# Performance work log

Hardware: AMD Instinct MI355X
Metric: run time of the kernel (lower is better)

## Reference

```python
import jax, jax.numpy as jnp
import numpy as np

N_NODES = 100000
N_EDGES = 3200000
F_IN = 512
HIDDEN = 16
N_CLASSES = 7


def setup_inputs() -> dict:
    key = jax.random.key(0)
    k = jax.random.split(key, 6)
    x = jax.random.normal(k[0], (N_NODES, F_IN), dtype=jnp.float32)
    edge_index = jax.random.randint(k[1], (2, N_EDGES), 0, N_NODES, dtype=jnp.int32)
    W1 = jax.random.normal(k[2], (F_IN, HIDDEN), dtype=jnp.float32) / np.sqrt(F_IN)
    b1 = jnp.zeros((HIDDEN,), dtype=jnp.float32)
    W2 = jax.random.normal(k[3], (HIDDEN, N_CLASSES), dtype=jnp.float32) / np.sqrt(HIDDEN)
    b2 = jnp.zeros((N_CLASSES,), dtype=jnp.float32)
    return {"x": x, "edge_index": edge_index, "W1": W1, "b1": b1, "W2": W2, "b2": b2}


def _gcn_norm(edge_index, num_nodes):
    # gcn_norm with add_self_loops=True, edge_weight=None (all ones).
    loops = jnp.arange(num_nodes, dtype=edge_index.dtype)
    row = jnp.concatenate([edge_index[0], loops])  # source
    col = jnp.concatenate([edge_index[1], loops])  # target
    w = jnp.ones(row.shape[0], dtype=jnp.float32)
    deg = jax.ops.segment_sum(w, col, num_segments=num_nodes)  # in-degree
    dinv = jnp.where(deg > 0, jax.lax.rsqrt(deg), 0.0)
    norm = dinv[row] * dinv[col]  # D^{-1/2} A D^{-1/2}
    return row, col, norm


def _gcn_conv(h, row, col, norm, W, b, num_nodes):
    h = h @ W  # transform first (out_channels small)
    msg = norm[:, None] * h[row]  # gather + scale over edges
    out = jax.ops.segment_sum(msg, col, num_segments=num_nodes)  # scatter-add
    return out + b


def reference(x, edge_index, W1, b1, W2, b2):
    n = x.shape[0]
    row, col, norm = _gcn_norm(edge_index, n)
    h = jax.nn.relu(_gcn_conv(x, row, col, norm, W1, b1, n))
    # dropout is identity in eval mode (training=False)
    return _gcn_conv(h, row, col, norm, W2, b2, n)
```

## Files before the change

### kernel.cpp

```cpp
#include <hip/hip_runtime.h>
#include <hip/hip_fp16.h>

#define F_IN 512
#define HID  16
#define NCLS 7
#define BSH  8
#define NPB  256
#define MAXBKT 1024
#define GRID_P 512


__global__ void k_zero(int* __restrict__ p, int m) {
    int i = blockIdx.x * blockDim.x + threadIdx.x;
    if (i < m) p[i] = 0;
}

__global__ void k_bhist(const int* __restrict__ dst, int* __restrict__ bcnt,
                        int E, int nbkt, int chunk) {
    __shared__ int h[MAXBKT];
    for (int i = threadIdx.x; i < nbkt; i += blockDim.x) h[i] = 0;
    __syncthreads();
    int base = blockIdx.x * chunk;
    int end = min(base + chunk, E);
    for (int e = base + threadIdx.x; e < end; e += blockDim.x)
        atomicAdd(&h[((unsigned)dst[e]) >> BSH], 1);
    __syncthreads();
    for (int i = threadIdx.x; i < nbkt; i += blockDim.x)
        if (h[i]) atomicAdd(&bcnt[i * 16], h[i]);
}

__global__ void k_bscan(const int* __restrict__ bcnt, int* __restrict__ bptr,
                        int* __restrict__ bcur, int nbkt) {
    __shared__ int s[1024];
    int tid = threadIdx.x;
    int v = (tid < nbkt) ? bcnt[tid * 16] : 0;
    s[tid] = v;
    __syncthreads();
    for (int off = 1; off < 1024; off <<= 1) {
        int t = (tid >= off) ? s[tid - off] : 0;
        __syncthreads();
        if (tid >= off) s[tid] += t;
        __syncthreads();
    }
    if (tid < nbkt) {
        int e = s[tid] - v;
        bptr[tid] = e;
        bcur[tid * 16] = e;
    }
}

__global__ void k_part(const int* __restrict__ ei, int* __restrict__ bcur,
                       unsigned* __restrict__ pairs, int E, int nbkt, int chunk) {
    __shared__ int h[MAXBKT];
    __shared__ int cur[MAXBKT];
    int tid = threadIdx.x;
    for (int i = tid; i < nbkt; i += blockDim.x) h[i] = 0;
    __syncthreads();
    int base = blockIdx.x * chunk;
    int end = min(base + chunk, E);
    for (int e = base + tid; e < end; e += blockDim.x)
        atomicAdd(&h[((unsigned)ei[E + e]) >> BSH], 1);
    __syncthreads();
    for (int i = tid; i < nbkt; i += blockDim.x) {
        int c = h[i];
        cur[i] = c ? atomicAdd(&bcur[i * 16], c) : 0;
    }
    __syncthreads();
    for (int e = base + tid; e < end; e += blockDim.x) {
        int d = ei[E + e];
        int b = ((unsigned)d) >> BSH;
        int pos = atomicAdd(&cur[b], 1);
        pairs[pos] = (((unsigned)ei[e]) << BSH) | (unsigned)(d & (NPB - 1));
    }
}

__global__ __launch_bounds__(NPB) void k_bfill(
    const unsigned* __restrict__ pairs, const int* __restrict__ bptr,
    int* __restrict__ row_ptr, int* __restrict__ srcarr,
    float* __restrict__ dinv, int n, int E, int nbkt) {
    int b = blockIdx.x, tid = threadIdx.x;
    int pb = bptr[b];
    int pe = (b + 1 < nbkt) ? bptr[b + 1] : E;
    __shared__ int h[NPB];
    __shared__ int s[NPB];
    h[tid] = 0;
    __syncthreads();
    for (int p = pb + tid; p < pe; p += NPB)
        atomicAdd(&h[pairs[p] & (NPB - 1)], 1);
    __syncthreads();
    int cnt = h[tid];
    s[tid] = cnt;
    __syncthreads();
    for (int off = 1; off < NPB; off <<= 1) {
        int t = (tid >= off) ? s[tid - off] : 0;
        __syncthreads();
        if (tid >= off) s[tid] += t;
        __syncthreads();
    }
    int excl = s[tid] - cnt;
    int node = (b << BSH) + tid;
    if (node < n) {
        row_ptr[node] = pb + excl;
        dinv[node] = rsqrtf((float)(cnt + 1));
    }
    h[tid] = pb + excl;
    __syncthreads();
    for (int p = pb + tid; p < pe; p += NPB) {
        unsigned v = pairs[p];
        int pos = atomicAdd(&h[v & (NPB - 1)], 1);
        srcarr[pos] = (int)(v >> BSH);
    }
    if (b == 0 && tid == 0) row_ptr[n] = E;
}


__global__ __launch_bounds__(256) void k_gemm1(const float* __restrict__ x,
                                               const float* __restrict__ W1,
                                               __half* __restrict__ h1, int n) {
    int node = blockIdx.x * blockDim.x + threadIdx.x;
    if (node >= n) return;
    float acc[HID];
#pragma unroll
    for (int j = 0; j < HID; j++) acc[j] = 0.f;
    const float* xr = x + (size_t)node * F_IN;
    for (int k0 = 0; k0 < F_IN; k0 += 32) {
        float4 xv[8];
        const float4* xp = (const float4*)(xr + k0);
#pragma unroll
        for (int u = 0; u < 8; u++) xv[u] = xp[u];
#pragma unroll
        for (int u = 0; u < 8; u++) {
#pragma unroll
            for (int kk = 0; kk < 4; kk++) {
                float xk = ((const float*)&xv[u])[kk];
                const float* wr = W1 + (size_t)(k0 + u * 4 + kk) * HID;
#pragma unroll
                for (int j = 0; j < HID; j++) acc[j] = fmaf(xk, wr[j], acc[j]);
            }
        }
    }
    __half2 hp[8];
#pragma unroll
    for (int j = 0; j < 8; j++)
        hp[j] = __float22half2_rn(float2{acc[2 * j], acc[2 * j + 1]});
    float4* o4 = (float4*)(h1 + (size_t)node * HID);
    o4[0] = *(float4*)&hp[0];
    o4[1] = *(float4*)&hp[4];
}

__device__ __forceinline__ void acc_row16(const __half* __restrict__ h1, int r,
                                          float nm, float* acc) {
    const float4* hr = (const float4*)(h1 + (size_t)r * HID);
    float4 raw0 = hr[0], raw1 = hr[1];
    const __half2* p0 = (const __half2*)&raw0;
    const __half2* p1 = (const __half2*)&raw1;
#pragma unroll
    for (int j = 0; j < 4; j++) {
        float2 f0 = __half22float2(p0[j]);
        float2 f1 = __half22float2(p1[j]);
        acc[2 * j + 0] = fmaf(nm, f0.x, acc[2 * j + 0]);
        acc[2 * j + 1] = fmaf(nm, f0.y, acc[2 * j + 1]);
        acc[8 + 2 * j + 0] = fmaf(nm, f1.x, acc[8 + 2 * j + 0]);
        acc[8 + 2 * j + 1] = fmaf(nm, f1.y, acc[8 + 2 * j + 1]);
    }
}

__global__ __launch_bounds__(256) void k_gather1(
    const int* __restrict__ row_ptr, const int* __restrict__ srcarr,
    const float* __restrict__ dinv, const __half* __restrict__ h1,
    const float* __restrict__ b1, const float* __restrict__ W2,
    __half* __restrict__ t, int n) {
    int g = blockIdx.x * blockDim.x + threadIdx.x;
    int node = g >> 2, q = g & 3;
    if (node >= n) return;
    int eb = row_ptr[node], ee = row_ptr[node + 1];
    float dc = dinv[node];
    float acc[HID];
#pragma unroll
    for (int j = 0; j < HID; j++) acc[j] = 0.f;
    int e = eb + q;
    for (; e + 4 < ee; e += 8) {
        int r0 = srcarr[e], r1 = srcarr[e + 4];
        float nm0 = dinv[r0] * dc, nm1 = dinv[r1] * dc;
        acc_row16(h1, r0, nm0, acc);
        acc_row16(h1, r1, nm1, acc);
    }
    if (e < ee) {
        int r0 = srcarr[e];
        acc_row16(h1, r0, dinv[r0] * dc, acc);
    }
#pragma unroll
    for (int m = 1; m < 4; m <<= 1)
#pragma unroll
        for (int j = 0; j < HID; j++) acc[j] += __shfl_xor(acc[j], m, 4);
    float d2 = dc * dc;
    float z[HID];
    {
        const float4* hs4 = (const float4*)(h1 + (size_t)node * HID);
        float4 raw0 = hs4[0], raw1 = hs4[1];
        const __half2* p0 = (const __half2*)&raw0;
        const __half2* p1 = (const __half2*)&raw1;
#pragma unroll
        for (int j = 0; j < 4; j++) {
            float2 f0 = __half22float2(p0[j]);
            float2 f1 = __half22float2(p1[j]);
            z[2 * j + 0] = fmaxf(fmaf(d2, f0.x, acc[2 * j + 0]) + b1[2 * j + 0], 0.f);
            z[2 * j + 1] = fmaxf(fmaf(d2, f0.y, acc[2 * j + 1]) + b1[2 * j + 1], 0.f);
            z[8 + 2 * j + 0] = fmaxf(fmaf(d2, f1.x, acc[8 + 2 * j + 0]) + b1[8 + 2 * j + 0], 0.f);
            z[8 + 2 * j + 1] = fmaxf(fmaf(d2, f1.y, acc[8 + 2 * j + 1]) + b1[8 + 2 * j + 1], 0.f);
        }
    }
    int j0 = q * 2, j1 = q * 2 + 1;
    float t0 = 0.f, t1 = 0.f;
#pragma unroll
    for (int k = 0; k < HID; k++) {
        t0 = fmaf(z[k], W2[k * NCLS + j0], t0);
        if (j1 < NCLS) t1 = fmaf(z[k], W2[k * NCLS + j1], t1);
    }
    if (j1 >= NCLS) t1 = 0.f;
    ((__half2*)t)[(size_t)node * 4 + q] = __float22half2_rn(float2{t0, t1});
}

__global__ __launch_bounds__(256) void k_gather2(
    const int* __restrict__ row_ptr, const int* __restrict__ srcarr,
    const float* __restrict__ dinv, const __half* __restrict__ t,
    const float* __restrict__ b2, float* __restrict__ out, int n) {
    int g = blockIdx.x * blockDim.x + threadIdx.x;
    int node = g >> 2, q = g & 3;
    if (node >= n) return;
    int eb = row_ptr[node], ee = row_ptr[node + 1];
    float dc = dinv[node];
    float acc[8];
#pragma unroll
    for (int j = 0; j < 8; j++) acc[j] = 0.f;
    const float4* t4 = (const float4*)t;
    int e = eb + q;
    for (; e + 4 < ee; e += 8) {
        int r0 = srcarr[e], r1 = srcarr[e + 4];
        float nm0 = dinv[r0] * dc, nm1 = dinv[r1] * dc;
        float4 raw0 = t4[r0], raw1 = t4[r1];
        const __half2* p0 = (const __half2*)&raw0;
        const __half2* p1 = (const __half2*)&raw1;
#pragma unroll
        for (int j = 0; j < 4; j++) {
            float2 f0 = __half22float2(p0[j]);
            float2 f1 = __half22float2(p1[j]);
            acc[2 * j + 0] = fmaf(nm0, f0.x, acc[2 * j + 0]);
            acc[2 * j + 1] = fmaf(nm0, f0.y, acc[2 * j + 1]);
            acc[2 * j + 0] = fmaf(nm1, f1.x, acc[2 * j + 0]);
            acc[2 * j + 1] = fmaf(nm1, f1.y, acc[2 * j + 1]);
        }
    }
    if (e < ee) {
        int r0 = srcarr[e];
        float nm0 = dinv[r0] * dc;
        float4 raw0 = t4[r0];
        const __half2* p0 = (const __half2*)&raw0;
#pragma unroll
        for (int j = 0; j < 4; j++) {
            float2 f0 = __half22float2(p0[j]);
            acc[2 * j + 0] = fmaf(nm0, f0.x, acc[2 * j + 0]);
            acc[2 * j + 1] = fmaf(nm0, f0.y, acc[2 * j + 1]);
        }
    }
#pragma unroll
    for (int m = 1; m < 4; m <<= 1)
#pragma unroll
        for (int j = 0; j < 8; j++) acc[j] += __shfl_xor(acc[j], m, 4);
    float d2 = dc * dc;
    float4 raws = t4[node];
    const __half2* ps = (const __half2*)&raws;
    float self[8];
#pragma unroll
    for (int j = 0; j < 4; j++) {
        float2 f = __half22float2(ps[j]);
        self[2 * j] = f.x;
        self[2 * j + 1] = f.y;
    }
    int j0 = q * 2, j1 = q * 2 + 1;
    float* o = out + (size_t)node * NCLS;
    o[j0] = fmaf(d2, self[j0], acc[j0]) + b2[j0];
    if (j1 < NCLS) o[j1] = fmaf(d2, self[j1], acc[j1]) + b2[j1];
}

extern "C" void kernel_launch(void* const* d_in, const int* in_sizes, int n_in,
                              void* d_out, int out_size, void* d_ws, size_t ws_size,
                              hipStream_t stream) {
    const float* x  = (const float*)d_in[0];
    const int*   ei = (const int*)d_in[1];
    const float* W1 = (const float*)d_in[2];
    const float* b1 = (const float*)d_in[3];
    const float* W2 = (const float*)d_in[4];
    const float* b2 = (const float*)d_in[5];
    float* out = (float*)d_out;

    int n = in_sizes[0] / F_IN;
    int E = in_sizes[1] / 2;
    int nbkt = (n + NPB - 1) >> BSH;

    float* ws = (float*)d_ws;
    float* dinv    = ws;
    int*   row_ptr = (int*)(ws + n);
    int*   srcarr  = (int*)(ws + 2 * (size_t)n + 4);
    float* R       = ws + 2 * (size_t)n + 4 + E;
    unsigned* pairs = (unsigned*)R;
    __half* h1     = (__half*)R;
    __half* t      = (__half*)(R + 8 * (size_t)n);
    int*   bcnt    = (int*)(R + E);
    int*   bptr    = bcnt + 1024 * 16;
    int*   bcur    = bptr + 1024;

    const int B = 256;
    int chunk = (E + GRID_P - 1) / GRID_P;

    k_zero<<<dim3((1024 * 16 + B - 1) / B), dim3(B), 0, stream>>>(bcnt, 1024 * 16);
    k_bhist<<<dim3(GRID_P), dim3(B), 0, stream>>>(ei + E, bcnt, E, nbkt, chunk);
    k_bscan<<<dim3(1), dim3(1024), 0, stream>>>(bcnt, bptr, bcur, nbkt);
    k_part<<<dim3(GRID_P), dim3(B), 0, stream>>>(ei, bcur, pairs, E, nbkt, chunk);
    k_bfill<<<dim3(nbkt), dim3(NPB), 0, stream>>>(pairs, bptr, row_ptr, srcarr, dinv, n, E, nbkt);
    k_gemm1<<<dim3((n + B - 1) / B), dim3(B), 0, stream>>>(x, W1, h1, n);
    k_gather1<<<dim3((n * 4 + B - 1) / B), dim3(B), 0, stream>>>(row_ptr, srcarr, dinv, h1, b1, W2, t, n);
    k_gather2<<<dim3((n * 4 + B - 1) / B), dim3(B), 0, stream>>>(row_ptr, srcarr, dinv, t, b2, out, n);
}
```

Baseline: 524.0 us.

## Overlap GEMM1 with CSR build kernels and pre-scale features by dinv

Splits the dense X·W1 GEMM across extra blocks appended to the histogram, partition and fill kernels, so the GEMM runs alongside the graph-structure build instead of as a separate launch. A new scale kernel multiplies h1 by dinv per source node. The gathers then become plain sums with one dc factor at the end, which removes the per-edge dinv[r] gather. Gather loops are also unrolled to four edges per iteration, and the workspace no longer aliases pairs with h1, which costs more memory.

```diff
diff --git a/kernel.cpp b/kernel.cpp
--- a/kernel.cpp
+++ b/kernel.cpp
@@ -9,15 +9,56 @@
 #define MAXBKT 1024
 #define GRID_P 512
 
+__device__ __forceinline__ void gemm1_block(const float* __restrict__ x,
+                                            const float* __restrict__ W1,
+                                            __half* __restrict__ h1, int n,
+                                            int vblk, int tid) {
+    int node = vblk * 256 + tid;
+    if (node >= n) return;
+    float acc[HID];
+#pragma unroll
+    for (int j = 0; j < HID; j++) acc[j] = 0.f;
+    const float* xr = x + (size_t)node * F_IN;
+    for (int k0 = 0; k0 < F_IN; k0 += 32) {
+        float4 xv[8];
+        const float4* xp = (const float4*)(xr + k0);
+#pragma unroll
+        for (int u = 0; u < 8; u++) xv[u] = xp[u];
+#pragma unroll
+        for (int u = 0; u < 8; u++) {
+#pragma unroll
+            for (int kk = 0; kk < 4; kk++) {
+                float xk = ((const float*)&xv[u])[kk];
+                const float* wr = W1 + (size_t)(k0 + u * 4 + kk) * HID;
+#pragma unroll
+                for (int j = 0; j < HID; j++) acc[j] = fmaf(xk, wr[j], acc[j]);
+            }
+        }
+    }
+    __half2 hp[8];
+#pragma unroll
+    for (int j = 0; j < 8; j++)
+        hp[j] = __float22half2_rn(float2{acc[2 * j], acc[2 * j + 1]});
+    float4* o4 = (float4*)(h1 + (size_t)node * HID);
+    o4[0] = *(float4*)&hp[0];
+    o4[1] = *(float4*)&hp[4];
+}
+
 
 __global__ void k_zero(int* __restrict__ p, int m) {
     int i = blockIdx.x * blockDim.x + threadIdx.x;
     if (i < m) p[i] = 0;
 }
 
-__global__ void k_bhist(const int* __restrict__ dst, int* __restrict__ bcnt,
-                        int E, int nbkt, int chunk) {
+__global__ __launch_bounds__(256) void k_bhist_gemm(
+    const int* __restrict__ dst, int* __restrict__ bcnt, int E, int nbkt, int chunk,
+    const float* __restrict__ x, const float* __restrict__ W1,
+    __half* __restrict__ h1, int n) {
     __shared__ int h[MAXBKT];
+    if (blockIdx.x >= GRID_P) {
+        gemm1_block(x, W1, h1, n, (int)blockIdx.x - GRID_P, threadIdx.x);
+        return;
+    }
     for (int i = threadIdx.x; i < nbkt; i += blockDim.x) h[i] = 0;
     __syncthreads();
     int base = blockIdx.x * chunk;
@@ -49,10 +90,17 @@
     }
 }
 
-__global__ void k_part(const int* __restrict__ ei, int* __restrict__ bcur,
-                       unsigned* __restrict__ pairs, int E, int nbkt, int chunk) {
+__global__ __launch_bounds__(256) void k_part_gemm(
+    const int* __restrict__ ei, int* __restrict__ bcur,
+    unsigned* __restrict__ pairs, int E, int nbkt, int chunk,
+    const float* __restrict__ x, const float* __restrict__ W1,
+    __half* __restrict__ h1, int n, int gbase) {
     __shared__ int h[MAXBKT];
     __shared__ int cur[MAXBKT];
+    if (blockIdx.x >= GRID_P) {
+        gemm1_block(x, W1, h1, n, gbase + (int)blockIdx.x - GRID_P, threadIdx.x);
+        return;
+    }
     int tid = threadIdx.x;
     for (int i = tid; i < nbkt; i += blockDim.x) h[i] = 0;
     __syncthreads();
@@ -74,15 +122,21 @@
     }
 }
 
-__global__ __launch_bounds__(NPB) void k_bfill(
+__global__ __launch_bounds__(NPB) void k_bfill_gemm(
     const unsigned* __restrict__ pairs, const int* __restrict__ bptr,
     int* __restrict__ row_ptr, int* __restrict__ srcarr,
-    float* __restrict__ dinv, int n, int E, int nbkt) {
+    float* __restrict__ dinv, int n, int E, int nbkt,
+    const float* __restrict__ x, const float* __restrict__ W1,
+    __half* __restrict__ h1, int gbase) {
+    __shared__ int h[NPB];
+    __shared__ int s[NPB];
     int b = blockIdx.x, tid = threadIdx.x;
+    if (b >= nbkt) {
+        gemm1_block(x, W1, h1, n, gbase + b - nbkt, tid);
+        return;
+    }
     int pb = bptr[b];
     int pe = (b + 1 < nbkt) ? bptr[b + 1] : E;
-    __shared__ int h[NPB];
-    __shared__ int s[NPB];
     h[tid] = 0;
     __syncthreads();
     for (int p = pb + tid; p < pe; p += NPB)
@@ -114,42 +168,28 @@
 }
 
 
-__global__ __launch_bounds__(256) void k_gemm1(const float* __restrict__ x,
-                                               const float* __restrict__ W1,
-                                               __half* __restrict__ h1, int n) {
-    int node = blockIdx.x * blockDim.x + threadIdx.x;
-    if (node >= n) return;
-    float acc[HID];
-#pragma unroll
-    for (int j = 0; j < HID; j++) acc[j] = 0.f;
-    const float* xr = x + (size_t)node * F_IN;
-    for (int k0 = 0; k0 < F_IN; k0 += 32) {
-        float4 xv[8];
-        const float4* xp = (const float4*)(xr + k0);
-#pragma unroll
-        for (int u = 0; u < 8; u++) xv[u] = xp[u];
-#pragma unroll
-        for (int u = 0; u < 8; u++) {
-#pragma unroll
-            for (int kk = 0; kk < 4; kk++) {
-                float xk = ((const float*)&xv[u])[kk];
-                const float* wr = W1 + (size_t)(k0 + u * 4 + kk) * HID;
-#pragma unroll
-                for (int j = 0; j < HID; j++) acc[j] = fmaf(xk, wr[j], acc[j]);
-            }
-        }
-    }
-    __half2 hp[8];
-#pragma unroll
-    for (int j = 0; j < 8; j++)
-        hp[j] = __float22half2_rn(float2{acc[2 * j], acc[2 * j + 1]});
-    float4* o4 = (float4*)(h1 + (size_t)node * HID);
-    o4[0] = *(float4*)&hp[0];
-    o4[1] = *(float4*)&hp[4];
-}
-
-__device__ __forceinline__ void acc_row16(const __half* __restrict__ h1, int r,
-                                          float nm, float* acc) {
+__global__ __launch_bounds__(256) void k_scale(__half* __restrict__ h1,
+                                               const float* __restrict__ dinv, int n) {
+    int i = blockIdx.x * blockDim.x + threadIdx.x;
+    if (i >= n) return;
+    float d = dinv[i];
+    float4* p = (float4*)(h1 + (size_t)i * HID);
+    float4 a = p[0], b = p[1];
+    __half2* ha = (__half2*)&a;
+    __half2* hb = (__half2*)&b;
+#pragma unroll
+    for (int j = 0; j < 4; j++) {
+        float2 f = __half22float2(ha[j]);
+        ha[j] = __float22half2_rn(float2{f.x * d, f.y * d});
+        f = __half22float2(hb[j]);
+        hb[j] = __float22half2_rn(float2{f.x * d, f.y * d});
+    }
+    p[0] = a;
+    p[1] = b;
+}
+
+__device__ __forceinline__ void add_row16(const __half* __restrict__ h1, int r,
+                                          float* acc) {
     const float4* hr = (const float4*)(h1 + (size_t)r * HID);
     float4 raw0 = hr[0], raw1 = hr[1];
     const __half2* p0 = (const __half2*)&raw0;
@@ -158,10 +198,10 @@
     for (int j = 0; j < 4; j++) {
         float2 f0 = __half22float2(p0[j]);
         float2 f1 = __half22float2(p1[j]);
-        acc[2 * j + 0] = fmaf(nm, f0.x, acc[2 * j + 0]);
-        acc[2 * j + 1] = fmaf(nm, f0.y, acc[2 * j + 1]);
-        acc[8 + 2 * j + 0] = fmaf(nm, f1.x, acc[8 + 2 * j + 0]);
-        acc[8 + 2 * j + 1] = fmaf(nm, f1.y, acc[8 + 2 * j + 1]);
+        acc[2 * j + 0] += f0.x;
+        acc[2 * j + 1] += f0.y;
+        acc[8 + 2 * j + 0] += f1.x;
+        acc[8 + 2 * j + 1] += f1.y;
     }
 }
 
@@ -179,21 +219,23 @@
 #pragma unroll
     for (int j = 0; j < HID; j++) acc[j] = 0.f;
     int e = eb + q;
+    for (; e + 12 < ee; e += 16) {
+        int r0 = srcarr[e], r1 = srcarr[e + 4], r2 = srcarr[e + 8], r3 = srcarr[e + 12];
+        add_row16(h1, r0, acc);
+        add_row16(h1, r1, acc);
+        add_row16(h1, r2, acc);
+        add_row16(h1, r3, acc);
+    }
     for (; e + 4 < ee; e += 8) {
         int r0 = srcarr[e], r1 = srcarr[e + 4];
-        float nm0 = dinv[r0] * dc, nm1 = dinv[r1] * dc;
-        acc_row16(h1, r0, nm0, acc);
-        acc_row16(h1, r1, nm1, acc);
-    }
-    if (e < ee) {
-        int r0 = srcarr[e];
-        acc_row16(h1, r0, dinv[r0] * dc, acc);
-    }
+        add_row16(h1, r0, acc);
+        add_row16(h1, r1, acc);
+    }
+    if (e < ee) add_row16(h1, srcarr[e], acc);
 #pragma unroll
     for (int m = 1; m < 4; m <<= 1)
 #pragma unroll
         for (int j = 0; j < HID; j++) acc[j] += __shfl_xor(acc[j], m, 4);
-    float d2 = dc * dc;
     float z[HID];
     {
         const float4* hs4 = (const float4*)(h1 + (size_t)node * HID);
@@ -204,10 +246,10 @@
         for (int j = 0; j < 4; j++) {
             float2 f0 = __half22float2(p0[j]);
             float2 f1 = __half22float2(p1[j]);
-            z[2 * j + 0] = fmaxf(fmaf(d2, f0.x, acc[2 * j + 0]) + b1[2 * j + 0], 0.f);
-            z[2 * j + 1] = fmaxf(fmaf(d2, f0.y, acc[2 * j + 1]) + b1[2 * j + 1], 0.f);
-            z[8 + 2 * j + 0] = fmaxf(fmaf(d2, f1.x, acc[8 + 2 * j + 0]) + b1[8 + 2 * j + 0], 0.f);
-            z[8 + 2 * j + 1] = fmaxf(fmaf(d2, f1.y, acc[8 + 2 * j + 1]) + b1[8 + 2 * j + 1], 0.f);
+            z[2 * j + 0] = fmaxf(fmaf(dc, acc[2 * j + 0] + f0.x, b1[2 * j + 0]), 0.f);
+            z[2 * j + 1] = fmaxf(fmaf(dc, acc[2 * j + 1] + f0.y, b1[2 * j + 1]), 0.f);
+            z[8 + 2 * j + 0] = fmaxf(fmaf(dc, acc[8 + 2 * j + 0] + f1.x, b1[8 + 2 * j + 0]), 0.f);
+            z[8 + 2 * j + 1] = fmaxf(fmaf(dc, acc[8 + 2 * j + 1] + f1.y, b1[8 + 2 * j + 1]), 0.f);
         }
     }
     int j0 = q * 2, j1 = q * 2 + 1;
@@ -218,7 +260,21 @@
         if (j1 < NCLS) t1 = fmaf(z[k], W2[k * NCLS + j1], t1);
     }
     if (j1 >= NCLS) t1 = 0.f;
+    t0 *= dc;
+    t1 *= dc;
     ((__half2*)t)[(size_t)node * 4 + q] = __float22half2_rn(float2{t0, t1});
+}
+
+__device__ __forceinline__ void add_row8(const float4* __restrict__ t4, int r,
+                                         float* acc) {
+    float4 raw = t4[r];
+    const __half2* p = (const __half2*)&raw;
+#pragma unroll
+    for (int j = 0; j < 4; j++) {
+        float2 f = __half22float2(p[j]);
+        acc[2 * j + 0] += f.x;
+        acc[2 * j + 1] += f.y;
+    }
 }
 
 __global__ __launch_bounds__(256) void k_gather2(
@@ -235,39 +291,23 @@
     for (int j = 0; j < 8; j++) acc[j] = 0.f;
     const float4* t4 = (const float4*)t;
     int e = eb + q;
+    for (; e + 12 < ee; e += 16) {
+        int r0 = srcarr[e], r1 = srcarr[e + 4], r2 = srcarr[e + 8], r3 = srcarr[e + 12];
+        add_row8(t4, r0, acc);
+        add_row8(t4, r1, acc);
+        add_row8(t4, r2, acc);
+        add_row8(t4, r3, acc);
+    }
     for (; e + 4 < ee; e += 8) {
         int r0 = srcarr[e], r1 = srcarr[e + 4];
-        float nm0 = dinv[r0] * dc, nm1 = dinv[r1] * dc;
-        float4 raw0 = t4[r0], raw1 = t4[r1];
-        const __half2* p0 = (const __half2*)&raw0;
-        const __half2* p1 = (const __half2*)&raw1;
-#pragma unroll
-        for (int j = 0; j < 4; j++) {
-            float2 f0 = __half22float2(p0[j]);
-            float2 f1 = __half22float2(p1[j]);
-            acc[2 * j + 0] = fmaf(nm0, f0.x, acc[2 * j + 0]);
-            acc[2 * j + 1] = fmaf(nm0, f0.y, acc[2 * j + 1]);
-            acc[2 * j + 0] = fmaf(nm1, f1.x, acc[2 * j + 0]);
-            acc[2 * j + 1] = fmaf(nm1, f1.y, acc[2 * j + 1]);
-        }
-    }
-    if (e < ee) {
-        int r0 = srcarr[e];
-        float nm0 = dinv[r0] * dc;
-        float4 raw0 = t4[r0];
-        const __half2* p0 = (const __half2*)&raw0;
-#pragma unroll
-        for (int j = 0; j < 4; j++) {
-            float2 f0 = __half22float2(p0[j]);
-            acc[2 * j + 0] = fmaf(nm0, f0.x, acc[2 * j + 0]);
-            acc[2 * j + 1] = fmaf(nm0, f0.y, acc[2 * j + 1]);
-        }
-    }
+        add_row8(t4, r0, acc);
+        add_row8(t4, r1, acc);
+    }
+    if (e < ee) add_row8(t4, srcarr[e], acc);
 #pragma unroll
     for (int m = 1; m < 4; m <<= 1)
 #pragma unroll
         for (int j = 0; j < 8; j++) acc[j] += __shfl_xor(acc[j], m, 4);
-    float d2 = dc * dc;
     float4 raws = t4[node];
     const __half2* ps = (const __half2*)&raws;
     float self[8];
@@ -279,8 +319,8 @@
     }
     int j0 = q * 2, j1 = q * 2 + 1;
     float* o = out + (size_t)node * NCLS;
-    o[j0] = fmaf(d2, self[j0], acc[j0]) + b2[j0];
-    if (j1 < NCLS) o[j1] = fmaf(d2, self[j1], acc[j1]) + b2[j1];
+    o[j0] = fmaf(dc, acc[j0] + self[j0], b2[j0]);
+    if (j1 < NCLS) o[j1] = fmaf(dc, acc[j1] + self[j1], b2[j1]);
 }
 
 extern "C" void kernel_launch(void* const* d_in, const int* in_sizes, int n_in,
@@ -299,26 +339,37 @@
     int nbkt = (n + NPB - 1) >> BSH;
 
     float* ws = (float*)d_ws;
-    float* dinv    = ws;
-    int*   row_ptr = (int*)(ws + n);
-    int*   srcarr  = (int*)(ws + 2 * (size_t)n + 4);
-    float* R       = ws + 2 * (size_t)n + 4 + E;
-    unsigned* pairs = (unsigned*)R;
-    __half* h1     = (__half*)R;
-    __half* t      = (__half*)(R + 8 * (size_t)n);
-    int*   bcnt    = (int*)(R + E);
-    int*   bptr    = bcnt + 1024 * 16;
-    int*   bcur    = bptr + 1024;
+    size_t off = 0;
+    float* dinv    = ws + off;              off += (size_t)n;
+    int*   row_ptr = (int*)(ws + off);      off += (size_t)n + 4;
+    int*   srcarr  = (int*)(ws + off);      off += (size_t)E;
+    unsigned* pairs = (unsigned*)(ws + off); off += (size_t)E;
+    int*   bcnt    = (int*)(ws + off);      off += 1024 * 16;
+    int*   bptr    = (int*)(ws + off);      off += 1024;
+    int*   bcur    = (int*)(ws + off);      off += 1024 * 16;
+    off = (off + 3) & ~(size_t)3;
+    __half* h1     = (__half*)(ws + off);   off += 8 * (size_t)n;
+    off = (off + 3) & ~(size_t)3;
+    __half* t      = (__half*)(ws + off);
 
     const int B = 256;
     int chunk = (E + GRID_P - 1) / GRID_P;
 
+    int nb = (n + B - 1) / B;
+    int nbA = nb < 64 ? nb : 64;
+    int nbB = (nb - nbA) < 196 ? (nb - nbA) : 196;
+    int nbC = nb - nbA - nbB;
+
     k_zero<<<dim3((1024 * 16 + B - 1) / B), dim3(B), 0, stream>>>(bcnt, 1024 * 16);
-    k_bhist<<<dim3(GRID_P), dim3(B), 0, stream>>>(ei + E, bcnt, E, nbkt, chunk);
+    k_bhist_gemm<<<dim3(GRID_P + nbA), dim3(B), 0, stream>>>(ei + E, bcnt, E, nbkt, chunk,
+                                                             x, W1, h1, n);
     k_bscan<<<dim3(1), dim3(1024), 0, stream>>>(bcnt, bptr, bcur, nbkt);
-    k_part<<<dim3(GRID_P), dim3(B), 0, stream>>>(ei, bcur, pairs, E, nbkt, chunk);
-    k_bfill<<<dim3(nbkt), dim3(NPB), 0, stream>>>(pairs, bptr, row_ptr, srcarr, dinv, n, E, nbkt);
-    k_gemm1<<<dim3((n + B - 1) / B), dim3(B), 0, stream>>>(x, W1, h1, n);
+    k_part_gemm<<<dim3(GRID_P + nbB), dim3(B), 0, stream>>>(ei, bcur, pairs, E, nbkt, chunk,
+                                                            x, W1, h1, n, nbA);
+    k_bfill_gemm<<<dim3(nbkt + nbC), dim3(NPB), 0, stream>>>(pairs, bptr, row_ptr, srcarr,
+                                                             dinv, n, E, nbkt,
+                                                             x, W1, h1, nbA + nbB);
+    k_scale<<<dim3(nb), dim3(B), 0, stream>>>(h1, dinv, n);
     k_gather1<<<dim3((n * 4 + B - 1) / B), dim3(B), 0, stream>>>(row_ptr, srcarr, dinv, h1, b1, W2, t, n);
     k_gather2<<<dim3((n * 4 + B - 1) / B), dim3(B), 0, stream>>>(row_ptr, srcarr, dinv, t, b2, out, n);
 }
```

Result: faster. 493.4 us (-5.8%).
